# Kernel optimization log

Hardware: AMD Instinct MI355X
Metric: run time of the kernel (lower is better)

The kernel has to match this reference:

```python
import jax, jax.numpy as jnp
import numpy as np

N = 768
D = 128
H0 = 256                      # int(256*sqrt(1))
H1 = 362                      # int(256*sqrt(2))


def _infonce(x, y, W1, b1, W2, b2):
    """InfoNCE lower bound with a Linear-ReLU-Linear critic.

    torch computes F(cat(x_tile, y_tile)) on all N^2 pairs where
    T1[j, i] = F(cat(x[i], y[j])). We split W1 into its x- and y- blocks so
    the first GEMM runs on N rows instead of N^2 (identical math), then
    broadcast-add before the ReLU.
    """
    dx = x.shape[1]
    hx = x @ W1[:dx]            # [N, h]
    hy = y @ W1[dx:]            # [N, h]
    # positives: aligned pairs (i == j)
    t0 = jax.nn.relu(hx + hy + b1) @ W2 + b2          # [N, 1]
    # all pairs: h[j, i] = relu(hx[i] + hy[j] + b1)
    h = jax.nn.relu(hx[None, :, :] + hy[:, None, :] + b1)   # [N, N, h]
    t1 = jnp.einsum('jih,ho->ji', h, W2) + b2[0]             # [N, N]
    lse = jax.nn.logsumexp(t1, axis=1)                        # [N]
    n = x.shape[0]
    return t0.mean() - (lse.mean() - jnp.log(jnp.asarray(n, x.dtype)))


def setup_inputs() -> dict:
    key = jax.random.key(0)
    ks = jax.random.split(key, 8)
    s = 0.05
    return {
        's0': jax.random.normal(ks[0], (N, D), jnp.float32),
        's1': jax.random.normal(ks[1], (N, D), jnp.float32),
        's2': jax.random.normal(ks[2], (N, D), jnp.float32),
        'W1_0': jax.random.normal(ks[3], (2 * D, H0), jnp.float32) * s,
        'b1_0': jnp.zeros((H0,), jnp.float32),
        'W2_0': jax.random.normal(ks[4], (H0, 1), jnp.float32) * s,
        'b2_0': jnp.zeros((1,), jnp.float32),
        'W1_1': jax.random.normal(ks[5], (3 * D, H1), jnp.float32) * s,
        'b1_1': jnp.zeros((H1,), jnp.float32),
        'W2_1': jax.random.normal(ks[6], (H1, 1), jnp.float32) * s,
        'b2_1': jnp.zeros((1,), jnp.float32),
    }


def reference(s0, s1, s2, W1_0, b1_0, W2_0, b2_0, W1_1, b1_1, W2_1, b2_1):
    # TCLineEstimator.forward: sum of chained InfoNCE bounds
    #   I(s0; s1) + I([s0, s1]; s2)
    mi0 = _infonce(s0, s1, W1_0, b1_0, W2_0, b2_0)
    cat01 = jnp.concatenate([s0, s1], axis=1)
    mi1 = _infonce(cat01, s2, W1_1, b1_1, W2_1, b2_1)
    return mi0 + mi1
```

## Files before the change

kernel.cpp:

```cpp
#include <hip/hip_runtime.h>
#include <math.h>

#define NROW 768
#define DIM  128

constexpr int H0c  = 256;
constexpr int H1c  = 362;
constexpr int HP1c = 368;

constexpr int HX0_OFF  = 0;
constexpr int HYB0_OFF = 196608;
constexpr int HX1_OFF  = 393216;
constexpr int HYB1_OFF = 675840;
constexpr int PMAX_OFF = 958464;
constexpr int PSUM_OFF = 964608;
constexpr int DIAG_OFF = 970752;
constexpr int UHP_OFF  = 972288;

template <int M, int HT>
__device__ __forceinline__ void prep_body(
    const float* __restrict__ s0, const float* __restrict__ s1, const float* __restrict__ s2,
    const float* __restrict__ W1_0, const float* __restrict__ b1_0, const float* __restrict__ W2_0,
    const float* __restrict__ W1_1, const float* __restrict__ b1_1, const float* __restrict__ W2_1,
    float* __restrict__ ws, float* __restrict__ xs) {
  constexpr int K     = (M == 2) ? 256 : 128;
  constexpr int HREAL = (M <= 1) ? H0c : H1c;
  constexpr int HP    = (M <= 1) ? H0c : HP1c;
  constexpr int WOFF  = (M == 1) ? 128 : (M == 3) ? 256 : 0;
  constexpr int HACT  = (M <= 1) ? 256 : 184;
  constexpr int EST   = (M <= 1) ? 0 : 1;

  const float* __restrict__ W    = (M <= 1) ? W1_0 : W1_1;
  const float* __restrict__ bias = (M == 1) ? b1_0 : (M == 3) ? b1_1 : nullptr;
  const float* __restrict__ W2   = (M <= 1) ? W2_0 : W2_1;

  const int i0  = blockIdx.x * 16;
  const int tx  = threadIdx.x;
  const int ty  = threadIdx.y;
  const int tid = ty * 64 + tx;

  {
    const float* __restrict__ sa = (M == 3) ? s2 : (M == 1) ? s1 : s0;
    constexpr int NF4 = 16 * (K / 4);
    for (int idx = tid; idx < NF4; idx += 256) {
      const int row = idx / (K / 4);
      const int c4  = (idx % (K / 4)) * 4;
      float4 v;
      if (M == 2 && c4 >= DIM)
        v = *(const float4*)&s1[(i0 + row) * DIM + (c4 - DIM)];
      else
        v = *(const float4*)&sa[(i0 + row) * DIM + c4];
      *(float4*)&xs[row * K + c4] = v;
    }
  }
  __syncthreads();

  const bool own   = (tx * 4 < HACT);
  const int  h4    = HT * HACT + tx * 4;
  const bool fullw = (h4 + 4 <= HREAL);
  const int  h4c   = fullw ? h4 : (HREAL - 4);
  const int  r0    = ty * 4;
  float acc[4][4] = {};
  const float* __restrict__ Wb = W + WOFF * HREAL + h4c;

  for (int d = 0; d < K; d += 4) {
    float4 xv[4];
    #pragma unroll
    for (int r = 0; r < 4; ++r) xv[r] = *(const float4*)&xs[(r0 + r) * K + d];
    float4 wv[4];
    #pragma unroll
    for (int dd = 0; dd < 4; ++dd)
      wv[dd] = *(const float4*)&Wb[(d + dd) * HREAL];
    #pragma unroll
    for (int dd = 0; dd < 4; ++dd) {
      #pragma unroll
      for (int r = 0; r < 4; ++r) {
        const float xval = ((const float*)&xv[r])[dd];
        acc[r][0] = fmaf(xval, wv[dd].x, acc[r][0]);
        acc[r][1] = fmaf(xval, wv[dd].y, acc[r][1]);
        acc[r][2] = fmaf(xval, wv[dd].z, acc[r][2]);
        acc[r][3] = fmaf(xval, wv[dd].w, acc[r][3]);
      }
    }
  }

  if (M >= 2 && !fullw && h4 < HREAL) {
    #pragma unroll
    for (int r = 0; r < 4; ++r) {
      acc[r][0] = acc[r][2]; acc[r][1] = acc[r][3];
      acc[r][2] = 0.f;       acc[r][3] = 0.f;
    }
  }

  const bool ok0 = (h4 + 0 < HREAL), ok1 = (h4 + 1 < HREAL),
             ok2 = (h4 + 2 < HREAL), ok3 = (h4 + 3 < HREAL);

  float* __restrict__ outp = ws + ((M == 0) ? HX0_OFF : (M == 1) ? HYB0_OFF
                                 : (M == 2) ? HX1_OFF : HYB1_OFF);
  if (own && h4 < HP) {
    if ((M & 1) == 0) {
      const int pbase = (h4 >> 2) * (NROW * 4);
      #pragma unroll
      for (int r = 0; r < 4; ++r) {
        float4 v;
        v.x = ok0 ? acc[r][0] : 0.f;
        v.y = ok1 ? acc[r][1] : 0.f;
        v.z = ok2 ? acc[r][2] : 0.f;
        v.w = ok3 ? acc[r][3] : 0.f;
        *(float4*)&outp[pbase + (i0 + r0 + r) * 4] = v;
      }
    } else {
      float bv[4] = {0.f, 0.f, 0.f, 0.f};
      if (ok0) bv[0] = bias[h4 + 0];
      if (ok1) bv[1] = bias[h4 + 1];
      if (ok2) bv[2] = bias[h4 + 2];
      if (ok3) bv[3] = bias[h4 + 3];
      #pragma unroll
      for (int r = 0; r < 4; ++r) {
        float4 v;
        v.x = ok0 ? acc[r][0] + bv[0] : 0.f;
        v.y = ok1 ? acc[r][1] + bv[1] : 0.f;
        v.z = ok2 ? acc[r][2] + bv[2] : 0.f;
        v.w = ok3 ? acc[r][3] + bv[3] : 0.f;
        *(float4*)&outp[(i0 + r0 + r) * HP + h4] = v;
      }
    }
  }

  if ((M & 1) == 0) {
    float w2v[4];
    w2v[0] = (own && ok0) ? W2[h4 + 0] : 0.f;
    w2v[1] = (own && ok1) ? W2[h4 + 1] : 0.f;
    w2v[2] = (own && ok2) ? W2[h4 + 2] : 0.f;
    w2v[3] = (own && ok3) ? W2[h4 + 3] : 0.f;
    #pragma unroll
    for (int r = 0; r < 4; ++r) {
      float p = acc[r][0] * w2v[0] + acc[r][1] * w2v[1] +
                acc[r][2] * w2v[2] + acc[r][3] * w2v[3];
      #pragma unroll
      for (int off = 32; off > 0; off >>= 1) p += __shfl_xor(p, off);
      if (tx == 0)
        ws[UHP_OFF + EST * 1536 + HT * NROW + i0 + r0 + r] = p;
    }
  }
}

__global__ __launch_bounds__(256) void prep_kernel(
    const float* __restrict__ s0, const float* __restrict__ s1, const float* __restrict__ s2,
    const float* __restrict__ W1_0, const float* __restrict__ b1_0, const float* __restrict__ W2_0,
    const float* __restrict__ W1_1, const float* __restrict__ b1_1, const float* __restrict__ W2_1,
    float* __restrict__ ws) {
  __shared__ float xs[16 * 256];
  switch (blockIdx.y) {
    case 0: prep_body<0, 0>(s0, s1, s2, W1_0, b1_0, W2_0, W1_1, b1_1, W2_1, ws, xs); break;
    case 1: prep_body<1, 0>(s0, s1, s2, W1_0, b1_0, W2_0, W1_1, b1_1, W2_1, ws, xs); break;
    case 2: prep_body<2, 0>(s0, s1, s2, W1_0, b1_0, W2_0, W1_1, b1_1, W2_1, ws, xs); break;
    case 3: prep_body<2, 1>(s0, s1, s2, W1_0, b1_0, W2_0, W1_1, b1_1, W2_1, ws, xs); break;
    case 4: prep_body<3, 0>(s0, s1, s2, W1_0, b1_0, W2_0, W1_1, b1_1, W2_1, ws, xs); break;
    default: prep_body<3, 1>(s0, s1, s2, W1_0, b1_0, W2_0, W1_1, b1_1, W2_1, ws, xs); break;
  }
}

template <int HP, int HREAL, bool TWO>
__device__ __forceinline__ void pair_body(
    const float* __restrict__ hx4, const float* __restrict__ hyb,
    const float* __restrict__ W2, const float* __restrict__ uhp,
    float* __restrict__ pmax, float* __restrict__ psum, float* __restrict__ sdiag,
    float* sh) {
  constexpr int NQ = HP / 4;
  float* ys   = sh;
  float* w2s  = sh + 4 * HP;
  float* redm = w2s + HP;
  float* reds = redm + 16;

  const int tid = threadIdx.x;
  const int j0  = blockIdx.x * 4;
  const int iq  = blockIdx.y;
  const int i   = iq * 256 + tid;

  for (int idx = tid; idx < 4 * NQ; idx += 256) {
    const int row = idx / NQ;
    const int c4  = (idx % NQ) * 4;
    *(float4*)&ys[row * HP + c4] = *(const float4*)&hyb[(j0 + row) * HP + c4];
  }
  for (int q = tid; q < NQ; q += 256) {
    const int h = q * 4;
    float4 v;
    v.x = (h + 0 < HREAL) ? W2[h + 0] : 0.f;
    v.y = (h + 1 < HREAL) ? W2[h + 1] : 0.f;
    v.z = (h + 2 < HREAL) ? W2[h + 2] : 0.f;
    v.w = (h + 3 < HREAL) ? W2[h + 3] : 0.f;
    *(float4*)&w2s[h] = v;
  }
  __syncthreads();

  float u = uhp[i];
  if (TWO) u += uhp[NROW + i];
  u *= 0.5f;

  float acc[4] = {0.f, 0.f, 0.f, 0.f};
  const float* xp = hx4 + i * 4;
  #pragma unroll 2
  for (int hb = 0; hb < HP; hb += 4, xp += NROW * 4) {
    const float4 a = *(const float4*)xp;
    const float4 w = *(const float4*)&w2s[hb];
    #pragma unroll
    for (int r = 0; r < 4; ++r) {
      const float4 y = *(const float4*)&ys[r * HP + hb];
      acc[r] = fmaf(fabsf(a.x + y.x), w.x, acc[r]);
      acc[r] = fmaf(fabsf(a.y + y.y), w.y, acc[r]);
      acc[r] = fmaf(fabsf(a.z + y.z), w.z, acc[r]);
      acc[r] = fmaf(fabsf(a.w + y.w), w.w, acc[r]);
    }
  }

  float s[4];
  #pragma unroll
  for (int r = 0; r < 4; ++r) s[r] = fmaf(0.5f, acc[r], u);

  const int dj = i - j0;
  if (dj == 0) sdiag[i] = s[0];
  else if (dj == 1) sdiag[i] = s[1];
  else if (dj == 2) sdiag[i] = s[2];
  else if (dj == 3) sdiag[i] = s[3];

  const int lane = tid & 63;
  const int wv   = tid >> 6;

  float M[4];
  #pragma unroll
  for (int r = 0; r < 4; ++r) {
    float mm = s[r];
    #pragma unroll
    for (int off = 32; off > 0; off >>= 1) mm = fmaxf(mm, __shfl_xor(mm, off));
    M[r] = mm;
  }
  if (lane == 0) {
    #pragma unroll
    for (int r = 0; r < 4; ++r) redm[wv * 4 + r] = M[r];
  }
  __syncthreads();
  #pragma unroll
  for (int r = 0; r < 4; ++r)
    M[r] = fmaxf(fmaxf(redm[r], redm[4 + r]), fmaxf(redm[8 + r], redm[12 + r]));

  #pragma unroll
  for (int r = 0; r < 4; ++r) {
    float e = __expf(s[r] - M[r]);
    #pragma unroll
    for (int off = 32; off > 0; off >>= 1) e += __shfl_xor(e, off);
    if (lane == 0) reds[wv * 4 + r] = e;
  }
  __syncthreads();
  if (tid < 4) {
    const float m = fmaxf(fmaxf(redm[tid], redm[4 + tid]),
                          fmaxf(redm[8 + tid], redm[12 + tid]));
    const float sm = reds[tid] + reds[4 + tid] + reds[8 + tid] + reds[12 + tid];
    pmax[(j0 + tid) * 4 + iq] = m;
    psum[(j0 + tid) * 4 + iq] = sm;
  }
}

__global__ __launch_bounds__(256) void pair_kernel(
    float* __restrict__ ws, const float* __restrict__ W2_0, const float* __restrict__ W2_1) {
  __shared__ float sh[4 * HP1c + HP1c + 32];
  if (blockIdx.z == 0)
    pair_body<H0c, H0c, false>(ws + HX0_OFF, ws + HYB0_OFF, W2_0, ws + UHP_OFF,
                               ws + PMAX_OFF, ws + PSUM_OFF, ws + DIAG_OFF, sh);
  else
    pair_body<HP1c, H1c, true>(ws + HX1_OFF, ws + HYB1_OFF, W2_1, ws + UHP_OFF + 1536,
                               ws + PMAX_OFF + 3072, ws + PSUM_OFF + 3072,
                               ws + DIAG_OFF + NROW, sh);
}

__global__ __launch_bounds__(1024) void final_kernel(
    const float* __restrict__ ws, float* __restrict__ out) {
  __shared__ float red[1024];
  const int t = threadIdx.x;
  float val = 0.f;
  if (t < NROW) {
    #pragma unroll
    for (int est = 0; est < 2; ++est) {
      const float* pm = ws + PMAX_OFF + est * 3072 + t * 4;
      const float* ps = ws + PSUM_OFF + est * 3072 + t * 4;
      float M = fmaxf(fmaxf(pm[0], pm[1]), pm[2]);
      float S = ps[0] * __expf(pm[0] - M) + ps[1] * __expf(pm[1] - M) +
                ps[2] * __expf(pm[2] - M);
      float lse = M + logf(S);
      val += ws[DIAG_OFF + est * NROW + t] - lse;
    }
  }
  red[t] = val;
  __syncthreads();
  for (int sdown = 512; sdown > 0; sdown >>= 1) {
    if (t < sdown) red[t] += red[t + sdown];
    __syncthreads();
  }
  if (t == 0) out[0] = red[0] * (1.0f / (float)NROW) + 2.0f * logf((float)NROW);
}

extern "C" void kernel_launch(void* const* d_in, const int* in_sizes, int n_in,
                              void* d_out, int out_size, void* d_ws, size_t ws_size,
                              hipStream_t stream) {
  const float* s0   = (const float*)d_in[0];
  const float* s1   = (const float*)d_in[1];
  const float* s2   = (const float*)d_in[2];
  const float* W1_0 = (const float*)d_in[3];
  const float* b1_0 = (const float*)d_in[4];
  const float* W2_0 = (const float*)d_in[5];
  const float* W1_1 = (const float*)d_in[7];
  const float* b1_1 = (const float*)d_in[8];
  const float* W2_1 = (const float*)d_in[9];
  float* ws  = (float*)d_ws;
  float* out = (float*)d_out;

  hipLaunchKernelGGL(prep_kernel, dim3(48, 6), dim3(64, 4), 0, stream,
                     s0, s1, s2, W1_0, b1_0, W2_0, W1_1, b1_1, W2_1, ws);
  hipLaunchKernelGGL(pair_kernel, dim3(192, 3, 2), dim3(256), 0, stream,
                     ws, W2_0, W2_1);
  hipLaunchKernelGGL(final_kernel, dim3(1), dim3(1024), 0, stream, ws, out);
}
```

Measured before the change: 60.28 us.

## Read pair-kernel operands directly from global and rebalance j-tiles per estimator

The pair kernel no longer stages the hy rows and W2 into shared memory. It reads them directly through uniform global loads, with W2 pre-padded into the workspace by the prep kernel. Estimator 1 (H=368) now processes 3 j-rows per block over 256 x-blocks, while estimator 0 keeps 4 rows. This balances work per block, schedules the heavier estimator first, and removes a syncthreads and the shared-memory fill phase. The cost is relying on cache for the broadcast loads, plus 192 idle blocks that exit early.

New measurement: 75.21 us. +24.8%, slower.

```diff
diff --git a/kernel.cpp b/kernel.cpp
--- a/kernel.cpp
+++ b/kernel.cpp
@@ -16,6 +16,7 @@
 constexpr int PSUM_OFF = 964608;
 constexpr int DIAG_OFF = 970752;
 constexpr int UHP_OFF  = 972288;
+constexpr int W2P_OFF  = 975360;
 
 template <int M, int HT>
 __device__ __forceinline__ void prep_body(
@@ -151,6 +152,13 @@
     const float* __restrict__ W1_1, const float* __restrict__ b1_1, const float* __restrict__ W2_1,
     float* __restrict__ ws) {
   __shared__ float xs[16 * 256];
+  if (blockIdx.y == 0 && blockIdx.x == 0) {
+    const int t = threadIdx.y * 64 + threadIdx.x;
+    for (int h = t; h < HP1c; h += 256) {
+      ws[W2P_OFF + h]        = (h < H0c) ? W2_0[h] : 0.f;
+      ws[W2P_OFF + HP1c + h] = (h < H1c) ? W2_1[h] : 0.f;
+    }
+  }
   switch (blockIdx.y) {
     case 0: prep_body<0, 0>(s0, s1, s2, W1_0, b1_0, W2_0, W1_1, b1_1, W2_1, ws, xs); break;
     case 1: prep_body<1, 0>(s0, s1, s2, W1_0, b1_0, W2_0, W1_1, b1_1, W2_1, ws, xs); break;
@@ -161,52 +169,37 @@
   }
 }
 
-template <int HP, int HREAL, bool TWO>
+template <int HP, int HREAL, int J, bool TWO>
 __device__ __forceinline__ void pair_body(
     const float* __restrict__ hx4, const float* __restrict__ hyb,
-    const float* __restrict__ W2, const float* __restrict__ uhp,
+    const float* __restrict__ w2p, const float* __restrict__ uhp,
     float* __restrict__ pmax, float* __restrict__ psum, float* __restrict__ sdiag,
-    float* sh) {
-  constexpr int NQ = HP / 4;
-  float* ys   = sh;
-  float* w2s  = sh + 4 * HP;
-  float* redm = w2s + HP;
-  float* reds = redm + 16;
-
+    float* redm, float* reds) {
   const int tid = threadIdx.x;
-  const int j0  = blockIdx.x * 4;
+  const int j0  = blockIdx.x * J;
   const int iq  = blockIdx.y;
   const int i   = iq * 256 + tid;
-
-  for (int idx = tid; idx < 4 * NQ; idx += 256) {
-    const int row = idx / NQ;
-    const int c4  = (idx % NQ) * 4;
-    *(float4*)&ys[row * HP + c4] = *(const float4*)&hyb[(j0 + row) * HP + c4];
-  }
-  for (int q = tid; q < NQ; q += 256) {
-    const int h = q * 4;
-    float4 v;
-    v.x = (h + 0 < HREAL) ? W2[h + 0] : 0.f;
-    v.y = (h + 1 < HREAL) ? W2[h + 1] : 0.f;
-    v.z = (h + 2 < HREAL) ? W2[h + 2] : 0.f;
-    v.w = (h + 3 < HREAL) ? W2[h + 3] : 0.f;
-    *(float4*)&w2s[h] = v;
-  }
-  __syncthreads();
 
   float u = uhp[i];
   if (TWO) u += uhp[NROW + i];
   u *= 0.5f;
 
-  float acc[4] = {0.f, 0.f, 0.f, 0.f};
-  const float* xp = hx4 + i * 4;
-  #pragma unroll 2
+  float acc[J];
+  #pragma unroll
+  for (int r = 0; r < J; ++r) acc[r] = 0.f;
+
+  const float* __restrict__ xp = hx4 + i * 4;
+  const float* __restrict__ yr[J];
+  #pragma unroll
+  for (int r = 0; r < J; ++r) yr[r] = hyb + (j0 + r) * HP;
+
+  #pragma unroll 4
   for (int hb = 0; hb < HP; hb += 4, xp += NROW * 4) {
     const float4 a = *(const float4*)xp;
-    const float4 w = *(const float4*)&w2s[hb];
-    #pragma unroll
-    for (int r = 0; r < 4; ++r) {
-      const float4 y = *(const float4*)&ys[r * HP + hb];
+    const float4 w = *(const float4*)&w2p[hb];
+    #pragma unroll
+    for (int r = 0; r < J; ++r) {
+      const float4 y = *(const float4*)&yr[r][hb];
       acc[r] = fmaf(fabsf(a.x + y.x), w.x, acc[r]);
       acc[r] = fmaf(fabsf(a.y + y.y), w.y, acc[r]);
       acc[r] = fmaf(fabsf(a.z + y.z), w.z, acc[r]);
@@ -214,22 +207,21 @@
     }
   }
 
-  float s[4];
-  #pragma unroll
-  for (int r = 0; r < 4; ++r) s[r] = fmaf(0.5f, acc[r], u);
+  float s[J];
+  #pragma unroll
+  for (int r = 0; r < J; ++r) s[r] = fmaf(0.5f, acc[r], u);
 
   const int dj = i - j0;
-  if (dj == 0) sdiag[i] = s[0];
-  else if (dj == 1) sdiag[i] = s[1];
-  else if (dj == 2) sdiag[i] = s[2];
-  else if (dj == 3) sdiag[i] = s[3];
+  #pragma unroll
+  for (int r = 0; r < J; ++r)
+    if (dj == r) sdiag[i] = s[r];
 
   const int lane = tid & 63;
   const int wv   = tid >> 6;
 
-  float M[4];
-  #pragma unroll
-  for (int r = 0; r < 4; ++r) {
+  float M[J];
+  #pragma unroll
+  for (int r = 0; r < J; ++r) {
     float mm = s[r];
     #pragma unroll
     for (int off = 32; off > 0; off >>= 1) mm = fmaxf(mm, __shfl_xor(mm, off));
@@ -237,40 +229,45 @@
   }
   if (lane == 0) {
     #pragma unroll
-    for (int r = 0; r < 4; ++r) redm[wv * 4 + r] = M[r];
+    for (int r = 0; r < J; ++r) redm[wv * J + r] = M[r];
   }
   __syncthreads();
   #pragma unroll
-  for (int r = 0; r < 4; ++r)
-    M[r] = fmaxf(fmaxf(redm[r], redm[4 + r]), fmaxf(redm[8 + r], redm[12 + r]));
-
-  #pragma unroll
-  for (int r = 0; r < 4; ++r) {
+  for (int r = 0; r < J; ++r)
+    M[r] = fmaxf(fmaxf(redm[r], redm[J + r]), fmaxf(redm[2 * J + r], redm[3 * J + r]));
+
+  #pragma unroll
+  for (int r = 0; r < J; ++r) {
     float e = __expf(s[r] - M[r]);
     #pragma unroll
     for (int off = 32; off > 0; off >>= 1) e += __shfl_xor(e, off);
-    if (lane == 0) reds[wv * 4 + r] = e;
+    if (lane == 0) reds[wv * J + r] = e;
   }
   __syncthreads();
-  if (tid < 4) {
-    const float m = fmaxf(fmaxf(redm[tid], redm[4 + tid]),
-                          fmaxf(redm[8 + tid], redm[12 + tid]));
-    const float sm = reds[tid] + reds[4 + tid] + reds[8 + tid] + reds[12 + tid];
+  if (tid < J) {
+    const float m = fmaxf(fmaxf(redm[tid], redm[J + tid]),
+                          fmaxf(redm[2 * J + tid], redm[3 * J + tid]));
+    const float sm = reds[tid] + reds[J + tid] + reds[2 * J + tid] + reds[3 * J + tid];
     pmax[(j0 + tid) * 4 + iq] = m;
     psum[(j0 + tid) * 4 + iq] = sm;
   }
 }
 
 __global__ __launch_bounds__(256) void pair_kernel(
-    float* __restrict__ ws, const float* __restrict__ W2_0, const float* __restrict__ W2_1) {
-  __shared__ float sh[4 * HP1c + HP1c + 32];
-  if (blockIdx.z == 0)
-    pair_body<H0c, H0c, false>(ws + HX0_OFF, ws + HYB0_OFF, W2_0, ws + UHP_OFF,
-                               ws + PMAX_OFF, ws + PSUM_OFF, ws + DIAG_OFF, sh);
-  else
-    pair_body<HP1c, H1c, true>(ws + HX1_OFF, ws + HYB1_OFF, W2_1, ws + UHP_OFF + 1536,
-                               ws + PMAX_OFF + 3072, ws + PSUM_OFF + 3072,
-                               ws + DIAG_OFF + NROW, sh);
+    float* __restrict__ ws) {
+  __shared__ float redm[16], reds[16];
+  if (blockIdx.z == 0) {
+    pair_body<HP1c, H1c, 3, true>(
+        ws + HX1_OFF, ws + HYB1_OFF, ws + W2P_OFF + HP1c, ws + UHP_OFF + 1536,
+        ws + PMAX_OFF + 3072, ws + PSUM_OFF + 3072, ws + DIAG_OFF + NROW,
+        redm, reds);
+  } else {
+    if (blockIdx.x >= 192) return;
+    pair_body<H0c, H0c, 4, false>(
+        ws + HX0_OFF, ws + HYB0_OFF, ws + W2P_OFF, ws + UHP_OFF,
+        ws + PMAX_OFF, ws + PSUM_OFF, ws + DIAG_OFF,
+        redm, reds);
+  }
 }
 
 __global__ __launch_bounds__(1024) void final_kernel(
@@ -316,7 +313,6 @@
 
   hipLaunchKernelGGL(prep_kernel, dim3(48, 6), dim3(64, 4), 0, stream,
                      s0, s1, s2, W1_0, b1_0, W2_0, W1_1, b1_1, W2_1, ws);
-  hipLaunchKernelGGL(pair_kernel, dim3(192, 3, 2), dim3(256), 0, stream,
-                     ws, W2_0, W2_1);
+  hipLaunchKernelGGL(pair_kernel, dim3(256, 3, 2), dim3(256), 0, stream, ws);
   hipLaunchKernelGGL(final_kernel, dim3(1), dim3(1024), 0, stream, ws, out);
 }
```
